# Kernel optimization log

Hardware: AMD Instinct MI355X
Metric: run time of the kernel (lower is better)

The kernel has to match this reference:

```python
import jax, jax.numpy as jnp
import numpy as np

B, T, C = 2, 2048, 1024
H = 16
HD = C // H

def setup_inputs() -> dict:
    key = jax.random.key(0)
    ks = jax.random.split(key, 5)
    scale = 0.02
    return {
        "x": jax.random.normal(ks[0], (B, T, C), jnp.float32),
        "w_attn": jax.random.normal(ks[1], (3 * C, C), jnp.float32) * scale,
        "b_attn": jnp.zeros((3 * C,), jnp.float32),
        "w_proj": jax.random.normal(ks[2], (C, C), jnp.float32) * scale,
        "b_proj": jnp.zeros((C,), jnp.float32),
    }

def reference(x, w_attn, b_attn, w_proj, b_proj):
    Bx, Tx, Cx = x.shape
    # qkv projection (torch Linear: x @ W^T + b)
    qkv = x @ w_attn.T + b_attn                     # [B,T,3C]
    q, k, v = jnp.split(qkv, 3, axis=2)
    # [B,T,C] -> [B,H,T,hd]
    def to_heads(t):
        return t.reshape(Bx, Tx, H, HD).transpose(0, 2, 1, 3)
    q, k, v = to_heads(q), to_heads(k), to_heads(v)
    scores = jnp.einsum('bhqd,bhkd->bhqk', q, k) / np.sqrt(HD).astype(jnp.float32)
    causal_mask = jnp.triu(jnp.ones((Tx, Tx), bool), k=1)   # True above diagonal
    scores = jnp.where(causal_mask, -jnp.inf, scores)
    attn = jax.nn.softmax(scores, axis=-1)
    y = jnp.einsum('bhqk,bhkd->bhqd', attn, v)      # [B,H,T,hd]
    y = y.transpose(0, 2, 1, 3).reshape(Bx, Tx, Cx)
    return y @ w_proj.T + b_proj
```

## Files before the change

### kernel.cpp

```cpp
#include <hip/hip_runtime.h>
#include <hip/hip_bf16.h>

using bf16 = __hip_bfloat16;

typedef __bf16 bf16x8 __attribute__((ext_vector_type(8)));
typedef __bf16 bf16x4v __attribute__((ext_vector_type(4)));
typedef float  float4v __attribute__((ext_vector_type(4)));
typedef unsigned short u16x8 __attribute__((ext_vector_type(8)));

#define MFMA16x16x32(a, b, c) __builtin_amdgcn_mfma_f32_16x16x32_bf16((a), (b), (c), 0, 0, 0)

#if __has_builtin(__builtin_amdgcn_exp2f)
#define EXP2F(x) __builtin_amdgcn_exp2f(x)
#else
#define EXP2F(x) exp2f(x)
#endif

#define T_SEQ 2048
#define NHEAD 16
#define CDIM  1024
#define HD3   3072

__device__ __forceinline__ void async_copy16(const void* g, void* l) {
    __builtin_amdgcn_global_load_lds(
        (__attribute__((address_space(1))) unsigned int*)g,
        (__attribute__((address_space(3))) unsigned int*)l,
        16, 0, 0);
}

__global__ __launch_bounds__(256) void convert_detect_kernel(
    const float* __restrict__ x, const float* __restrict__ wa,
    const float* __restrict__ wp,
    bf16* __restrict__ xb, bf16* __restrict__ wab, bf16* __restrict__ wpb,
    int* __restrict__ flag)
{
    __shared__ int red[256];
    const u16x8* xs8 = (const u16x8*)x;
    int cnt = 0;
    for (int i = threadIdx.x; i < 2048; i += 256) {
        const u16x8 v = xs8[i];
#pragma unroll
        for (int t = 0; t < 8; ++t) {
            const int e = (v[t] >> 7) & 0xFF;
            if (e == 0xFF || (e != 0 && e < 0x60)) cnt++;
        }
    }
    red[threadIdx.x] = cnt;
    __syncthreads();
    for (int s = 128; s > 0; s >>= 1) {
        if (threadIdx.x < s) red[threadIdx.x] += red[threadIdx.x + s];
        __syncthreads();
    }
    const int isf32 = (red[0] > 100) ? 1 : 0;
    if (blockIdx.x == 0 && threadIdx.x == 0) flag[0] = isf32;
    if (!isf32) return;

    const int gid    = blockIdx.x * 256 + threadIdx.x;
    const int stride = gridDim.x * 256;
    const float4v* x4  = (const float4v*)x;
    const float4v* wa4 = (const float4v*)wa;
    const float4v* wp4 = (const float4v*)wp;
    bf16x4v* xb4  = (bf16x4v*)xb;
    bf16x4v* wab4 = (bf16x4v*)wab;
    bf16x4v* wpb4 = (bf16x4v*)wpb;

    for (int i = gid; i < 1048576; i += stride) {
        const float4v v = x4[i];
        bf16x4v o;
#pragma unroll
        for (int t = 0; t < 4; ++t) o[t] = (__bf16)v[t];
        xb4[i] = o;
    }
    for (int i = gid; i < 786432; i += stride) {
        const float4v v = wa4[i];
        bf16x4v o;
#pragma unroll
        for (int t = 0; t < 4; ++t) o[t] = (__bf16)v[t];
        wab4[i] = o;
    }
    for (int i = gid; i < 262144; i += stride) {
        const float4v v = wp4[i];
        bf16x4v o;
#pragma unroll
        for (int t = 0; t < 4; ++t) o[t] = (__bf16)v[t];
        wpb4[i] = o;
    }
}

template<int JF>
__global__ __launch_bounds__(256) void gemm_nt_lds_t(
    const void* __restrict__ Araw, const bf16* __restrict__ Aconv,
    const void* __restrict__ Braw, const bf16* __restrict__ Bconv,
    const void* __restrict__ biasraw, void* __restrict__ Cv,
    int M, int N, int K, const int* __restrict__ flag, int is_final,
    int scale_q, int swz)
{
    const bool f32 = (flag[0] != 0);
    const bf16* A = f32 ? Aconv : (const bf16*)Araw;
    const bf16* B = f32 ? Bconv : (const bf16*)Braw;

    __shared__ bf16 As[2][128 * 64];
    __shared__ bf16 Bs[2][JF * 32 * 64];

    const int tid  = threadIdx.x;
    const int lane = tid & 63;
    const int wave = tid >> 6;
    const int wm = wave & 1, wn = wave >> 1;
    const int c = lane & 15, g = lane >> 4;

    int bx = blockIdx.x, by = blockIdx.y;
    if (swz) {
        const int nwg = gridDim.x * gridDim.y;
        const int lin = by * gridDim.x + bx;
        const int nl  = (lin & 7) * (nwg >> 3) + (lin >> 3);
        bx = nl % gridDim.x;
        by = nl / gridDim.x;
    }
    const int bm = bx * 128;
    const int bn = by * (JF * 32);

    const int srow = tid >> 3;
    const int slc  = ((tid & 7) ^ (srow & 7)) * 8;
    const bf16* gA = A + (size_t)(bm + srow) * K + slc;
    const bf16* gB = B + (size_t)(bn + srow) * K + slc;

    float4v acc[4][JF] = {};

#pragma unroll
    for (int q = 0; q < 4; ++q)
        async_copy16(gA + (size_t)(q * 32) * K, &As[0][q * 2048 + tid * 8]);
#pragma unroll
    for (int q = 0; q < JF; ++q)
        async_copy16(gB + (size_t)(q * 32) * K, &Bs[0][q * 2048 + tid * 8]);
    __syncthreads();

    int b = 0;
    for (int k0 = 0; k0 < K; k0 += 64, b ^= 1) {
        if (k0 + 64 < K) {
#pragma unroll
            for (int q = 0; q < 4; ++q)
                async_copy16(gA + k0 + 64 + (size_t)(q * 32) * K,
                             &As[b ^ 1][q * 2048 + tid * 8]);
#pragma unroll
            for (int q = 0; q < JF; ++q)
                async_copy16(gB + k0 + 64 + (size_t)(q * 32) * K,
                             &Bs[b ^ 1][q * 2048 + tid * 8]);
        }

#pragma unroll
        for (int kk = 0; kk < 2; ++kk) {
            bf16x8 af[4], bfr[JF];
#pragma unroll
            for (int i = 0; i < 4; ++i)
                af[i]  = *(const bf16x8*)&As[b][(wm * 64 + i * 16 + c) * 64 +
                                               (((kk * 4 + g) ^ (c & 7)) * 8)];
#pragma unroll
            for (int j = 0; j < JF; ++j)
                bfr[j] = *(const bf16x8*)&Bs[b][(wn * (JF * 16) + j * 16 + c) * 64 +
                                               (((kk * 4 + g) ^ (c & 7)) * 8)];
#pragma unroll
            for (int i = 0; i < 4; ++i)
#pragma unroll
                for (int j = 0; j < JF; ++j)
                    acc[i][j] = MFMA16x16x32(af[i], bfr[j], acc[i][j]);
        }
        __syncthreads();
    }

    const bool f32o = is_final && f32;
    bf16*  Cb = (bf16*)Cv;
    float* Cf = (float*)Cv;

#pragma unroll
    for (int i = 0; i < 4; ++i) {
        const int row = bm + wm * 64 + i * 16 + g * 4;
#pragma unroll
        for (int j = 0; j < JF; ++j) {
            const int col = bn + wn * (JF * 16) + j * 16 + c;
            const float bv = f32 ? ((const float*)biasraw)[col]
                                 : __bfloat162float(((const bf16*)biasraw)[col]);
            const float sc = (scale_q && col < 1024) ? 0.18033688f : 1.0f;
            if (f32o) {
#pragma unroll
                for (int t = 0; t < 4; ++t)
                    Cf[(size_t)(row + t) * N + col] = (acc[i][j][t] + bv) * sc;
            } else {
#pragma unroll
                for (int t = 0; t < 4; ++t)
                    Cb[(size_t)(row + t) * N + col] =
                        __float2bfloat16((acc[i][j][t] + bv) * sc);
            }
        }
    }
}

__global__ __launch_bounds__(512) void attn_mfma(
    const bf16* __restrict__ qkv, bf16* __restrict__ y)
{
    __shared__ __bf16 Ks[2][128 * 64];
    __shared__ __bf16 Vt[2][64 * 128];

    const int tid  = threadIdx.x;
    const int lane = tid & 63;
    const int w    = tid >> 6;
    const int c    = lane & 15;
    const int g    = lane >> 4;

    const int i    = blockIdx.x;
    const int role = i >> 8;
    const int bhl  = i & 7;
    const int t5   = (i & 255) >> 3;
    const int j    = t5 >> 2;
    const int bh   = ((t5 & 3) << 3) | bhl;
    const int qblk = role ? j : (15 - j);
    const int bb   = bh >> 4;
    const int h    = bh & 15;
    const size_t base = (size_t)bb * T_SEQ * HD3 + (size_t)h * 64;

    const bool kstage = (tid < 256);
    const int st   = tid & 255;
    const int krow = st >> 3;
    const int klc  = ((st & 7) ^ (krow & 7)) * 8;
    const int kq   = st & 31;
    const int dgv  = st >> 5;
    const int vchunk = (kq >> 3) * 4 + (kq & 3);
    const int vlow   = ((kq >> 2) & 1) * 4;

    const bf16* kgbase = qkv + base + 1024;
    const bf16* vgbase = qkv + base + 2048;

    bf16x8 ones;
#pragma unroll
    for (int ii = 0; ii < 8; ++ii) ones[ii] = (__bf16)1.0f;

    const int q0 = qblk * 128;
    const int qw = q0 + w * 16;

    bf16x8 qf[2];
#pragma unroll
    for (int kf2 = 0; kf2 < 2; ++kf2)
        qf[kf2] = *(const bf16x8*)(qkv + base
            + (size_t)(qw + c) * HD3 + kf2 * 32 + g * 8);

    float4v o[4] = {};
    float4v ol = {};

    if (kstage) {
#pragma unroll
        for (int q = 0; q < 4; ++q)
            async_copy16(kgbase + (size_t)(q * 32 + krow) * HD3 + klc,
                         &Ks[0][q * 2048 + st * 8]);
    } else {
        bf16x8 vr[4];
#pragma unroll
        for (int r = 0; r < 4; ++r)
            vr[r] = *(const bf16x8*)(vgbase + (size_t)(kq * 4 + r) * HD3 + dgv * 8);
#pragma unroll
        for (int jj = 0; jj < 8; ++jj) {
            const int d = dgv * 8 + jj;
            bf16x4v pk;
#pragma unroll
            for (int r = 0; r < 4; ++r) pk[r] = vr[r][jj];
            *(bf16x4v*)&Vt[0][d * 128 + ((vchunk ^ (d & 7)) << 3) + vlow] = pk;
        }
    }
    __syncthreads();

    int b = 0;
    for (int kt = 0; kt <= q0; kt += 128, b ^= 1) {
        const bool more = (kt + 128 <= q0);
        bf16x8 vr[4];
        if (more) {
            if (kstage) {
#pragma unroll
                for (int q = 0; q < 4; ++q)
                    async_copy16(kgbase + (size_t)(kt + 128 + q * 32 + krow) * HD3 + klc,
                                 &Ks[b ^ 1][q * 2048 + st * 8]);
            } else {
#pragma unroll
                for (int r = 0; r < 4; ++r)
                    vr[r] = *(const bf16x8*)(vgbase + (size_t)(kt + 128 + kq * 4 + r) * HD3 + dgv * 8);
            }
        }

#pragma unroll
        for (int hf = 0; hf < 2; ++hf) {
            if (kt + hf * 64 > qw + 15) continue;

            float4v sacc[4] = {};
            __builtin_amdgcn_s_setprio(1);
#pragma unroll
            for (int jb = 0; jb < 4; ++jb) {
                const int key = hf * 64 + jb * 16 + c;
                bf16x8 a0 = *(const bf16x8*)&Ks[b][key * 64 + ((g ^ (c & 7)) * 8)];
                bf16x8 a1 = *(const bf16x8*)&Ks[b][key * 64 + (((4 + g) ^ (c & 7)) * 8)];
                sacc[jb] = MFMA16x16x32(a0, qf[0], sacc[jb]);
                sacc[jb] = MFMA16x16x32(a1, qf[1], sacc[jb]);
            }
            __builtin_amdgcn_s_setprio(0);

            bf16x8 pf[2];
            {
                if (kt + hf * 64 + 63 > qw) {
                    const int query = qw + c;
#pragma unroll
                    for (int jb = 0; jb < 4; ++jb) {
                        const int kb = kt + hf * 64 + jb * 16 + g * 4;
#pragma unroll
                        for (int t = 0; t < 4; ++t)
                            if (kb + t > query) sacc[jb][t] = -1e30f;
                    }
                }
#pragma unroll
                for (int jb = 0; jb < 4; ++jb)
#pragma unroll
                    for (int t = 0; t < 4; ++t)
                        sacc[jb][t] = EXP2F(sacc[jb][t]);
#pragma unroll
                for (int lkf = 0; lkf < 2; ++lkf) {
                    bf16x8 pk;
#pragma unroll
                    for (int jj = 0; jj < 8; ++jj)
                        pk[jj] = (__bf16)sacc[lkf * 2 + (jj >> 2)][jj & 3];
                    pf[lkf] = pk;
                }
            }

            __builtin_amdgcn_s_setprio(1);
#pragma unroll
            for (int lkf = 0; lkf < 2; ++lkf) {
                const int kf = hf * 2 + lkf;
                ol = MFMA16x16x32(ones, pf[lkf], ol);
#pragma unroll
                for (int dn = 0; dn < 4; ++dn) {
                    const int d = dn * 16 + c;
                    bf16x8 vf = *(const bf16x8*)
                        &Vt[b][d * 128 + (((kf * 4 + g) ^ (d & 7)) << 3)];
                    o[dn] = MFMA16x16x32(vf, pf[lkf], o[dn]);
                }
            }
            __builtin_amdgcn_s_setprio(0);
        }

        if (more && !kstage) {
#pragma unroll
            for (int jj = 0; jj < 8; ++jj) {
                const int d = dgv * 8 + jj;
                bf16x4v pk;
#pragma unroll
                for (int r = 0; r < 4; ++r) pk[r] = vr[r][jj];
                *(bf16x4v*)&Vt[b ^ 1][d * 128 + ((vchunk ^ (d & 7)) << 3) + vlow] = pk;
            }
        }
        __syncthreads();
    }

    {
        const float linv = 1.f / ol.x;
        const int q = qw + c;
        const size_t yb = ((size_t)bb * T_SEQ + q) * CDIM + h * 64;
#pragma unroll
        for (int dn = 0; dn < 4; ++dn) {
            bf16x4v ov;
#pragma unroll
            for (int t = 0; t < 4; ++t)
                ov[t] = (__bf16)(o[dn][t] * linv);
            *(bf16x4v*)&y[yb + dn * 16 + g * 4] = ov;
        }
    }
}

extern "C" void kernel_launch(void* const* d_in, const int* in_sizes, int n_in,
                              void* d_out, int out_size, void* d_ws, size_t ws_size,
                              hipStream_t stream)
{
    const int M = 4096;
    char* ws = (char*)d_ws;

    int*  flag = (int*)ws;
    bf16* xb   = (bf16*)(ws + 256);
    bf16* wab  = (bf16*)(ws + 8388864);
    bf16* wpb  = (bf16*)(ws + 14680320);
    bf16* qkv  = (bf16*)(ws + 16777472);
    bf16* yb   = (bf16*)(ws + 41943296);

    convert_detect_kernel<<<512, 256, 0, stream>>>(
        (const float*)d_in[0], (const float*)d_in[1], (const float*)d_in[3],
        xb, wab, wpb, flag);

    {
        dim3 grid(M / 128, 3072 / 64);
        gemm_nt_lds_t<2><<<grid, 256, 0, stream>>>(d_in[0], xb, d_in[1], wab,
                                                   d_in[2], qkv, M, 3072, 1024,
                                                   flag, 0, 1, 1);
    }
    {
        attn_mfma<<<512, 512, 0, stream>>>(qkv, yb);
    }
    {
        dim3 grid(M / 128, 1024 / 64);
        gemm_nt_lds_t<2><<<grid, 256, 0, stream>>>(yb, yb, d_in[3], wpb,
                                                   d_in[4], d_out, M, 1024, 1024,
                                                   flag, 1, 0, 1);
    }
    (void)in_sizes; (void)n_in; (void)out_size; (void)ws_size;
}
```

Baseline: 177.1 us.

## Fuse fp32-to-bf16 conversion of x into the QKV GEMM A-tile loader

Drops the separate pass that converted the activation x to bf16 in the workspace. The QKV GEMM now loads fp32 x through registers, converts to bf16 and writes it to LDS, prefetching the next tile while MFMAs run. This removes an extra read and write of x plus a buffer, but the A path loses its async global-to-LDS copies and adds register pressure and a convert step inside the main loop. The convert kernel grid is also halved.

```diff
diff --git a/kernel.cpp b/kernel.cpp
--- a/kernel.cpp
+++ b/kernel.cpp
@@ -31,7 +31,7 @@
 __global__ __launch_bounds__(256) void convert_detect_kernel(
     const float* __restrict__ x, const float* __restrict__ wa,
     const float* __restrict__ wp,
-    bf16* __restrict__ xb, bf16* __restrict__ wab, bf16* __restrict__ wpb,
+    bf16* __restrict__ wab, bf16* __restrict__ wpb,
     int* __restrict__ flag)
 {
     __shared__ int red[256];
@@ -57,20 +57,11 @@
 
     const int gid    = blockIdx.x * 256 + threadIdx.x;
     const int stride = gridDim.x * 256;
-    const float4v* x4  = (const float4v*)x;
     const float4v* wa4 = (const float4v*)wa;
     const float4v* wp4 = (const float4v*)wp;
-    bf16x4v* xb4  = (bf16x4v*)xb;
     bf16x4v* wab4 = (bf16x4v*)wab;
     bf16x4v* wpb4 = (bf16x4v*)wpb;
 
-    for (int i = gid; i < 1048576; i += stride) {
-        const float4v v = x4[i];
-        bf16x4v o;
-#pragma unroll
-        for (int t = 0; t < 4; ++t) o[t] = (__bf16)v[t];
-        xb4[i] = o;
-    }
     for (int i = gid; i < 786432; i += stride) {
         const float4v v = wa4[i];
         bf16x4v o;
@@ -89,15 +80,17 @@
 
 template<int JF>
 __global__ __launch_bounds__(256) void gemm_nt_lds_t(
-    const void* __restrict__ Araw, const bf16* __restrict__ Aconv,
+    const void* __restrict__ Araw,
     const void* __restrict__ Braw, const bf16* __restrict__ Bconv,
     const void* __restrict__ biasraw, void* __restrict__ Cv,
     int M, int N, int K, const int* __restrict__ flag, int is_final,
-    int scale_q, int swz)
+    int scale_q, int swz, int a_conv)
 {
-    const bool f32 = (flag[0] != 0);
-    const bf16* A = f32 ? Aconv : (const bf16*)Araw;
-    const bf16* B = f32 ? Bconv : (const bf16*)Braw;
+    const bool f32  = (flag[0] != 0);
+    const bool aF32 = f32 && (a_conv != 0);
+    const bf16*  Ab = (const bf16*)Araw;
+    const float* Af = (const float*)Araw;
+    const bf16*  B  = f32 ? Bconv : (const bf16*)Braw;
 
     __shared__ bf16 As[2][128 * 64];
     __shared__ bf16 Bs[2][JF * 32 * 64];
@@ -121,14 +114,32 @@
 
     const int srow = tid >> 3;
     const int slc  = ((tid & 7) ^ (srow & 7)) * 8;
-    const bf16* gA = A + (size_t)(bm + srow) * K + slc;
-    const bf16* gB = B + (size_t)(bn + srow) * K + slc;
+    const bf16* gA = Ab + (size_t)(bm + srow) * K + slc;
+    const bf16* gB = B  + (size_t)(bn + srow) * K + slc;
 
     float4v acc[4][JF] = {};
 
-#pragma unroll
-    for (int q = 0; q < 4; ++q)
-        async_copy16(gA + (size_t)(q * 32) * K, &As[0][q * 2048 + tid * 8]);
+    if (aF32) {
+        float4v ar[4][2];
+#pragma unroll
+        for (int q = 0; q < 4; ++q) {
+            const float* src = Af + (size_t)(bm + q * 32 + srow) * K + slc;
+            ar[q][0] = *(const float4v*)src;
+            ar[q][1] = *(const float4v*)(src + 4);
+        }
+#pragma unroll
+        for (int q = 0; q < 4; ++q) {
+            bf16x8 wv;
+#pragma unroll
+            for (int t = 0; t < 4; ++t) { wv[t] = (__bf16)ar[q][0][t];
+                                          wv[t + 4] = (__bf16)ar[q][1][t]; }
+            *(bf16x8*)&As[0][q * 2048 + tid * 8] = wv;
+        }
+    } else {
+#pragma unroll
+        for (int q = 0; q < 4; ++q)
+            async_copy16(gA + (size_t)(q * 32) * K, &As[0][q * 2048 + tid * 8]);
+    }
 #pragma unroll
     for (int q = 0; q < JF; ++q)
         async_copy16(gB + (size_t)(q * 32) * K, &Bs[0][q * 2048 + tid * 8]);
@@ -136,11 +147,24 @@
 
     int b = 0;
     for (int k0 = 0; k0 < K; k0 += 64, b ^= 1) {
-        if (k0 + 64 < K) {
-#pragma unroll
-            for (int q = 0; q < 4; ++q)
-                async_copy16(gA + k0 + 64 + (size_t)(q * 32) * K,
-                             &As[b ^ 1][q * 2048 + tid * 8]);
+        const bool more = (k0 + 64 < K);
+        float4v ar[4][2];
+
+        if (more) {
+            if (aF32) {
+#pragma unroll
+                for (int q = 0; q < 4; ++q) {
+                    const float* src = Af + (size_t)(bm + q * 32 + srow) * K
+                                          + (k0 + 64 + slc);
+                    ar[q][0] = *(const float4v*)src;
+                    ar[q][1] = *(const float4v*)(src + 4);
+                }
+            } else {
+#pragma unroll
+                for (int q = 0; q < 4; ++q)
+                    async_copy16(gA + k0 + 64 + (size_t)(q * 32) * K,
+                                 &As[b ^ 1][q * 2048 + tid * 8]);
+            }
 #pragma unroll
             for (int q = 0; q < JF; ++q)
                 async_copy16(gB + k0 + 64 + (size_t)(q * 32) * K,
@@ -163,6 +187,17 @@
 #pragma unroll
                 for (int j = 0; j < JF; ++j)
                     acc[i][j] = MFMA16x16x32(af[i], bfr[j], acc[i][j]);
+        }
+
+        if (more && aF32) {
+#pragma unroll
+            for (int q = 0; q < 4; ++q) {
+                bf16x8 wv;
+#pragma unroll
+                for (int t = 0; t < 4; ++t) { wv[t] = (__bf16)ar[q][0][t];
+                                              wv[t + 4] = (__bf16)ar[q][1][t]; }
+                *(bf16x8*)&As[b ^ 1][q * 2048 + tid * 8] = wv;
+            }
         }
         __syncthreads();
     }
@@ -378,30 +413,29 @@
     char* ws = (char*)d_ws;
 
     int*  flag = (int*)ws;
-    bf16* xb   = (bf16*)(ws + 256);
     bf16* wab  = (bf16*)(ws + 8388864);
     bf16* wpb  = (bf16*)(ws + 14680320);
     bf16* qkv  = (bf16*)(ws + 16777472);
     bf16* yb   = (bf16*)(ws + 41943296);
 
-    convert_detect_kernel<<<512, 256, 0, stream>>>(
+    convert_detect_kernel<<<256, 256, 0, stream>>>(
         (const float*)d_in[0], (const float*)d_in[1], (const float*)d_in[3],
-        xb, wab, wpb, flag);
+        wab, wpb, flag);
 
     {
         dim3 grid(M / 128, 3072 / 64);
-        gemm_nt_lds_t<2><<<grid, 256, 0, stream>>>(d_in[0], xb, d_in[1], wab,
+        gemm_nt_lds_t<2><<<grid, 256, 0, stream>>>(d_in[0], d_in[1], wab,
                                                    d_in[2], qkv, M, 3072, 1024,
-                                                   flag, 0, 1, 1);
+                                                   flag, 0, 1, 1, 1);
     }
     {
         attn_mfma<<<512, 512, 0, stream>>>(qkv, yb);
     }
     {
         dim3 grid(M / 128, 1024 / 64);
-        gemm_nt_lds_t<2><<<grid, 256, 0, stream>>>(yb, yb, d_in[3], wpb,
+        gemm_nt_lds_t<2><<<grid, 256, 0, stream>>>(yb, d_in[3], wpb,
                                                    d_in[4], d_out, M, 1024, 1024,
-                                                   flag, 1, 0, 1);
+                                                   flag, 1, 0, 1, 0);
     }
     (void)in_sizes; (void)n_in; (void)out_size; (void)ws_size;
 }
```

Result: slower. 209.5 us (+18.3%).
